# Performance work log

Hardware: AMD Instinct MI355X
Metric: run time of the kernel (lower is better)

## Reference

```python
import jax, jax.numpy as jnp
import numpy as np

BLOCK = 32          # per_1x32 microscaling block size along K
FP4_MAX = 6.0       # largest magnitude representable in e2m1
FP4_EMAX = 2.0      # exponent of largest fp4 binade (4..6)


def _quant_dequant_mxfp4(x):
    """Simulate MXFP4 (e2m1 elements, shared power-of-two E8M0 scale per 1x32
    block along the last dim): quantize then dequantize. x: [..., K], K % 32 == 0."""
    shape = x.shape
    xb = x.reshape(*shape[:-1], shape[-1] // BLOCK, BLOCK)
    amax = jnp.max(jnp.abs(xb), axis=-1, keepdims=True)
    # shared scale: 2^(floor(log2(amax)) - emax) so the block max lands in the top binade
    exp = jnp.floor(jnp.log2(jnp.maximum(amax, jnp.finfo(x.dtype).tiny))) - FP4_EMAX
    scale = jnp.where(amax > 0, jnp.exp2(exp), jnp.ones_like(amax))
    q = jnp.clip(xb / scale, -FP4_MAX, FP4_MAX)
    aq = jnp.abs(q)
    # e2m1 ulp: 0.5 on [0,2), 1 on [2,4), 2 on [4,6]
    lsb = jnp.where(aq < 2.0, 0.5, jnp.where(aq < 4.0, 1.0, 2.0))
    qr = jnp.round(q / lsb) * lsb  # round-to-nearest-even onto the fp4 grid
    return (qr * scale).reshape(shape)


def setup_inputs() -> dict:
    key = jax.random.key(0)
    k1, k2, k3 = jax.random.split(key, 3)
    B, S, K, N = 4, 2048, 2048, 2048
    inp = jax.random.normal(k1, (B, S, K), dtype=jnp.float32)
    weight = jax.random.normal(k2, (N, K), dtype=jnp.float32) * (1.0 / np.sqrt(K))
    bias = jax.random.normal(k3, (N,), dtype=jnp.float32) * 0.02
    return {"input": inp, "weight": weight, "bias": bias}


def reference(input, weight, bias):
    # both activation and weight are fake-quantized to MXFP4 per 1x32 blocks
    # along the contraction (in_features) dim, then a standard GEMM + bias.
    orig_shape = input.shape
    a = _quant_dequant_mxfp4(input.reshape(-1, orig_shape[-1]))  # [M, K]
    w = _quant_dequant_mxfp4(weight)                              # [N, K]
    out = jnp.einsum("mk,nk->mn", a, w) + bias
    return out.reshape(*orig_shape[:-1], weight.shape[0])
```

## Files before the change

### kernel.cpp

```cpp
#include <hip/hip_runtime.h>
#include <hip/hip_bf16.h>
#include <cstdint>


#define BM 128
#define BN 128
#define BKE 256

typedef float floatx4 __attribute__((ext_vector_type(4)));
typedef int intx8 __attribute__((ext_vector_type(8)));

#define GLOBAL_AS __attribute__((address_space(1)))
#define LDS_AS __attribute__((address_space(3)))


__device__ __forceinline__ int enc1(float x, float inv) {
    float q = x * inv;
    q = fminf(fmaxf(q, -6.0f), 6.0f);
    int s = (int)(__float_as_uint(q) >> 31) << 3;
    float aq = fabsf(q);
    float ilsb = aq < 2.0f ? 2.0f : (aq < 4.0f ? 1.0f : 0.5f);
    float lsb  = aq < 2.0f ? 0.5f : (aq < 4.0f ? 1.0f : 2.0f);
    float ar = rintf(aq * ilsb) * lsb;
    int c;
    if (ar < 2.0f)      c = (int)(ar * 2.0f);
    else if (ar < 4.0f) c = 2 + (int)ar;
    else                c = 4 + (int)(ar * 0.5f);
    return c | s;
}

__global__ void quant_mxfp4_v3(const float* __restrict__ A, uint8_t* __restrict__ Aq,
                               uint8_t* __restrict__ Asc,
                               const float* __restrict__ W, uint8_t* __restrict__ Wq,
                               uint8_t* __restrict__ Wsc,
                               long na4, long ntot4) {
    long t = (long)blockIdx.x * 256 + threadIdx.x;
    if (t >= ntot4) return;
    const float* src; uint8_t* dq; uint8_t* ds; long idx;
    if (t < na4) { src = A; dq = Aq; ds = Asc; idx = t; }
    else         { src = W; dq = Wq; ds = Wsc; idx = t - na4; }

    float4 f = ((const float4*)src)[idx];
    float amax = fmaxf(fmaxf(fabsf(f.x), fabsf(f.y)),
                       fmaxf(fabsf(f.z), fabsf(f.w)));
    amax = fmaxf(amax, __shfl_xor(amax, 1));
    amax = fmaxf(amax, __shfl_xor(amax, 2));
    amax = fmaxf(amax, __shfl_xor(amax, 4));

    int ebits = (int)((__float_as_uint(amax) >> 23) & 0xff);
    int sb;
    float inv;
    if (amax > 0.0f) {
        sb = ebits - 2; if (sb < 0) sb = 0;
        inv = __uint_as_float((unsigned)((256 - ebits) & 255) << 23);
    } else {
        sb = 127;
        inv = 0.0f;
    }

    int c0 = enc1(f.x, inv), c1 = enc1(f.y, inv);
    int c2 = enc1(f.z, inv), c3 = enc1(f.w, inv);
    ((unsigned short*)dq)[idx] =
        (unsigned short)(c0 | (c1 << 4) | (c2 << 8) | (c3 << 12));
    if ((idx & 7) == 0) ds[idx >> 3] = (uint8_t)sb;
}


__global__ void gemm_fp4_kernel(const uint8_t* __restrict__ Aq, const uint8_t* __restrict__ Asc,
                                const uint8_t* __restrict__ Wq, const uint8_t* __restrict__ Wsc,
                                const float* __restrict__ bias, float* __restrict__ C,
                                int M, int N, int K) {
    __shared__ __align__(16) uint8_t As4[BM * BKE / 2];
    __shared__ __align__(16) uint8_t Ws4[BN * BKE / 2];
    __shared__ __align__(16) uint8_t SAs[BM * 8];
    __shared__ __align__(16) uint8_t SWs[BN * 8];

    const int tid = threadIdx.x;
    const int lane = tid & 63;
    const int w = tid >> 6;
    const int wr = w >> 1;
    const int wc = w & 1;
    const int row16 = lane & 15;
    const int quad = lane >> 4;
    const int sh = quad * 8;
    const int m0 = blockIdx.y * BM;
    const int n0 = blockIdx.x * BN;
    const int KB2 = K >> 1, KB32 = K >> 5;

    floatx4 acc[4][4];
#pragma unroll
    for (int i = 0; i < 4; i++)
#pragma unroll
        for (int j = 0; j < 4; j++) acc[i][j] = (floatx4){0.f, 0.f, 0.f, 0.f};

    for (int k0 = 0; k0 < K; k0 += BKE) {
#pragma unroll
        for (int it = 0; it < 4; ++it) {
            int q = it * 256 + tid;
            int row = q >> 3, c = q & 7;
            int cg = c ^ (row & 7);
            const uint8_t* ga = Aq + (size_t)(m0 + row) * KB2 + (k0 >> 1) + cg * 16;
            __builtin_amdgcn_global_load_lds(
                (GLOBAL_AS void*)ga, (LDS_AS void*)(As4 + q * 16), 16, 0, 0);
        }
#pragma unroll
        for (int it = 0; it < 4; ++it) {
            int q = it * 256 + tid;
            int row = q >> 3, c = q & 7;
            int cg = c ^ (row & 7);
            const uint8_t* gw = Wq + (size_t)(n0 + row) * KB2 + (k0 >> 1) + cg * 16;
            __builtin_amdgcn_global_load_lds(
                (GLOBAL_AS void*)gw, (LDS_AS void*)(Ws4 + q * 16), 16, 0, 0);
        }
        {
            int row = tid >> 1, half = tid & 1;
            const uint8_t* gsa = Asc + (size_t)(m0 + row) * KB32 + (k0 >> 5) + half * 4;
            __builtin_amdgcn_global_load_lds(
                (GLOBAL_AS void*)gsa, (LDS_AS void*)(SAs + tid * 4), 4, 0, 0);
            const uint8_t* gsw = Wsc + (size_t)(n0 + row) * KB32 + (k0 >> 5) + half * 4;
            __builtin_amdgcn_global_load_lds(
                (GLOBAL_AS void*)gsw, (LDS_AS void*)(SWs + tid * 4), 4, 0, 0);
        }
        __syncthreads();

        uint2 sa2[4], sw2[4];
#pragma unroll
        for (int mi = 0; mi < 4; mi++)
            sa2[mi] = *(const uint2*)(SAs + (wr * 64 + mi * 16 + row16) * 8);
#pragma unroll
        for (int ni = 0; ni < 4; ni++)
            sw2[ni] = *(const uint2*)(SWs + (wc * 64 + ni * 16 + row16) * 8);

#pragma unroll
        for (int ks = 0; ks < 2; ++ks) {
            int4 af[4], wf[4];
#pragma unroll
            for (int mi = 0; mi < 4; mi++) {
                int r = wr * 64 + mi * 16 + row16;
                int c = ((ks * 4 + quad) ^ (r & 7)) * 16;
                af[mi] = *(const int4*)(As4 + r * 128 + c);
            }
#pragma unroll
            for (int ni = 0; ni < 4; ni++) {
                int r = wc * 64 + ni * 16 + row16;
                int c = ((ks * 4 + quad) ^ (r & 7)) * 16;
                wf[ni] = *(const int4*)(Ws4 + r * 128 + c);
            }
            int sas[4], sws[4];
#pragma unroll
            for (int mi = 0; mi < 4; mi++)
                sas[mi] = (int)(((ks ? sa2[mi].y : sa2[mi].x) >> sh) & 0xff);
#pragma unroll
            for (int ni = 0; ni < 4; ni++)
                sws[ni] = (int)(((ks ? sw2[ni].y : sw2[ni].x) >> sh) & 0xff);

#pragma unroll
            for (int mi = 0; mi < 4; mi++) {
                intx8 a8 = {af[mi].x, af[mi].y, af[mi].z, af[mi].w, 0, 0, 0, 0};
#pragma unroll
                for (int ni = 0; ni < 4; ni++) {
                    intx8 b8 = {wf[ni].x, wf[ni].y, wf[ni].z, wf[ni].w, 0, 0, 0, 0};
                    acc[mi][ni] = __builtin_amdgcn_mfma_scale_f32_16x16x128_f8f6f4(
                        a8, b8, acc[mi][ni], 4, 4, 0, sas[mi], 0, sws[ni]);
                }
            }
        }
        __syncthreads();
    }

#pragma unroll
    for (int ni = 0; ni < 4; ni++) {
        int n = n0 + wc * 64 + ni * 16 + row16;
        float bv = bias[n];
#pragma unroll
        for (int mi = 0; mi < 4; mi++) {
            int mbase = m0 + wr * 64 + mi * 16 + quad * 4;
#pragma unroll
            for (int r = 0; r < 4; r++) {
                C[(size_t)(mbase + r) * N + n] = acc[mi][ni][r] + bv;
            }
        }
    }
}


extern "C" void kernel_launch(void* const* d_in, const int* in_sizes, int n_in,
                              void* d_out, int out_size, void* d_ws, size_t ws_size,
                              hipStream_t stream) {
    const float* inp  = (const float*)d_in[0];
    const float* wgt  = (const float*)d_in[1];
    const float* bias = (const float*)d_in[2];
    float* out = (float*)d_out;

    const int N = in_sizes[2];
    const int K = in_sizes[1] / N;
    const long M = (long)in_sizes[0] / K;

    uint8_t* Aq4 = (uint8_t*)d_ws;
    uint8_t* Wq4 = Aq4 + (size_t)M * K / 2;
    uint8_t* Asc = Wq4 + (size_t)N * K / 2;
    uint8_t* Wsc = Asc + (size_t)M * K / 32;

    long na4   = (long)M * K / 4;
    long ntot4 = na4 + (long)N * K / 4;
    quant_mxfp4_v3<<<dim3((ntot4 + 255) / 256), dim3(256), 0, stream>>>(
        inp, Aq4, Asc, wgt, Wq4, Wsc, na4, ntot4);

    dim3 grid(N / BN, M / BM);
    gemm_fp4_kernel<<<grid, dim3(256), 0, stream>>>(
        Aq4, Asc, Wq4, Wsc, bias, out, (int)M, N, K);
}
```

Before: 158.2 us.

## Prepack FP4 operands in MFMA fragment order and load directly without LDS

The quantizer now writes FP4 values and scales in a tiled layout that matches the MFMA 16x16x128 lane order, one 1KB chunk per 16-row by 128-K tile. The GEMM drops shared memory and barriers and has each lane load its fragments and scales straight from global memory with contiguous 16-byte loads. This removes LDS staging and synchronization, but gives up reuse of tiles across waves through LDS. Each wave now reads its A and W tiles from global memory or L2 independently, with no software prefetch or double buffering. The layout math assumes K is a power of two divisible by 512.

```diff
diff --git a/kernel.cpp b/kernel.cpp
--- a/kernel.cpp
+++ b/kernel.cpp
@@ -3,15 +3,8 @@
 #include <cstdint>
 
 
-#define BM 128
-#define BN 128
-#define BKE 256
-
 typedef float floatx4 __attribute__((ext_vector_type(4)));
 typedef int intx8 __attribute__((ext_vector_type(8)));
-
-#define GLOBAL_AS __attribute__((address_space(1)))
-#define LDS_AS __attribute__((address_space(3)))
 
 
 __device__ __forceinline__ int enc1(float x, float inv) {
@@ -29,11 +22,11 @@
     return c | s;
 }
 
-__global__ void quant_mxfp4_v3(const float* __restrict__ A, uint8_t* __restrict__ Aq,
+__global__ void quant_mxfp4_v4(const float* __restrict__ A, uint8_t* __restrict__ Aq,
                                uint8_t* __restrict__ Asc,
                                const float* __restrict__ W, uint8_t* __restrict__ Wq,
                                uint8_t* __restrict__ Wsc,
-                               long na4, long ntot4) {
+                               long na4, long ntot4, int k4shift, int K) {
     long t = (long)blockIdx.x * 256 + threadIdx.x;
     if (t >= ntot4) return;
     const float* src; uint8_t* dq; uint8_t* ds; long idx;
@@ -60,21 +53,31 @@
 
     int c0 = enc1(f.x, inv), c1 = enc1(f.y, inv);
     int c2 = enc1(f.z, inv), c3 = enc1(f.w, inv);
-    ((unsigned short*)dq)[idx] =
+    unsigned short pk =
         (unsigned short)(c0 | (c1 << 4) | (c2 << 8) | (c3 << 12));
-    if ((idx & 7) == 0) ds[idx >> 3] = (uint8_t)sb;
+
+    int m = (int)(idx >> k4shift);
+    int k = (int)(idx & ((1 << k4shift) - 1)) << 2;
+    int KT = K >> 7;
+    int tm = m >> 4, tk = k >> 7;
+    int lane = (((k >> 5) & 3) << 4) | (m & 15);
+    size_t doff = (((size_t)tm * KT + tk) << 10) + (size_t)(lane << 4)
+                + (size_t)(((k & 31) >> 2) << 1);
+    *(unsigned short*)(dq + doff) = pk;
+
+    if ((k & 31) == 0) {
+        int KG = KT >> 2;
+        size_t soff = (((size_t)tm * KG + (tk >> 2)) << 8)
+                    + (size_t)(lane << 2) + (size_t)(tk & 3);
+        ds[soff] = (uint8_t)sb;
+    }
 }
 
 
-__global__ void gemm_fp4_kernel(const uint8_t* __restrict__ Aq, const uint8_t* __restrict__ Asc,
-                                const uint8_t* __restrict__ Wq, const uint8_t* __restrict__ Wsc,
-                                const float* __restrict__ bias, float* __restrict__ C,
-                                int M, int N, int K) {
-    __shared__ __align__(16) uint8_t As4[BM * BKE / 2];
-    __shared__ __align__(16) uint8_t Ws4[BN * BKE / 2];
-    __shared__ __align__(16) uint8_t SAs[BM * 8];
-    __shared__ __align__(16) uint8_t SWs[BN * 8];
-
+__global__ void gemm_fp4_flat(const uint8_t* __restrict__ Aq, const uint8_t* __restrict__ Asc,
+                              const uint8_t* __restrict__ Wq, const uint8_t* __restrict__ Wsc,
+                              const float* __restrict__ bias, float* __restrict__ C,
+                              int M, int N, int K) {
     const int tid = threadIdx.x;
     const int lane = tid & 63;
     const int w = tid >> 6;
@@ -82,10 +85,10 @@
     const int wc = w & 1;
     const int row16 = lane & 15;
     const int quad = lane >> 4;
-    const int sh = quad * 8;
-    const int m0 = blockIdx.y * BM;
-    const int n0 = blockIdx.x * BN;
-    const int KB2 = K >> 1, KB32 = K >> 5;
+    const int m0 = blockIdx.y * 128;
+    const int n0 = blockIdx.x * 128;
+    const int KT = K >> 7;
+    const int KG = KT >> 2;
 
     floatx4 acc[4][4];
 #pragma unroll
@@ -93,79 +96,55 @@
 #pragma unroll
         for (int j = 0; j < 4; j++) acc[i][j] = (floatx4){0.f, 0.f, 0.f, 0.f};
 
-    for (int k0 = 0; k0 < K; k0 += BKE) {
+    const uint8_t* aP[4];
+    const uint8_t* wP[4];
+    const uint8_t* aS[4];
+    const uint8_t* wS[4];
 #pragma unroll
-        for (int it = 0; it < 4; ++it) {
-            int q = it * 256 + tid;
-            int row = q >> 3, c = q & 7;
-            int cg = c ^ (row & 7);
-            const uint8_t* ga = Aq + (size_t)(m0 + row) * KB2 + (k0 >> 1) + cg * 16;
-            __builtin_amdgcn_global_load_lds(
-                (GLOBAL_AS void*)ga, (LDS_AS void*)(As4 + q * 16), 16, 0, 0);
-        }
+    for (int mi = 0; mi < 4; mi++) {
+        int tm = (m0 >> 4) + wr * 4 + mi;
+        aP[mi] = Aq + (((size_t)tm * KT) << 10) + (lane << 4);
+        aS[mi] = Asc + (((size_t)tm * KG) << 8) + (lane << 2);
+    }
 #pragma unroll
-        for (int it = 0; it < 4; ++it) {
-            int q = it * 256 + tid;
-            int row = q >> 3, c = q & 7;
-            int cg = c ^ (row & 7);
-            const uint8_t* gw = Wq + (size_t)(n0 + row) * KB2 + (k0 >> 1) + cg * 16;
-            __builtin_amdgcn_global_load_lds(
-                (GLOBAL_AS void*)gw, (LDS_AS void*)(Ws4 + q * 16), 16, 0, 0);
-        }
-        {
-            int row = tid >> 1, half = tid & 1;
-            const uint8_t* gsa = Asc + (size_t)(m0 + row) * KB32 + (k0 >> 5) + half * 4;
-            __builtin_amdgcn_global_load_lds(
-                (GLOBAL_AS void*)gsa, (LDS_AS void*)(SAs + tid * 4), 4, 0, 0);
-            const uint8_t* gsw = Wsc + (size_t)(n0 + row) * KB32 + (k0 >> 5) + half * 4;
-            __builtin_amdgcn_global_load_lds(
-                (GLOBAL_AS void*)gsw, (LDS_AS void*)(SWs + tid * 4), 4, 0, 0);
-        }
-        __syncthreads();
+    for (int ni = 0; ni < 4; ni++) {
+        int tn = (n0 >> 4) + wc * 4 + ni;
+        wP[ni] = Wq + (((size_t)tn * KT) << 10) + (lane << 4);
+        wS[ni] = Wsc + (((size_t)tn * KG) << 8) + (lane << 2);
+    }
 
-        uint2 sa2[4], sw2[4];
+    for (int g = 0; g < KG; ++g) {
+        unsigned int sa32[4], sw32[4];
 #pragma unroll
         for (int mi = 0; mi < 4; mi++)
-            sa2[mi] = *(const uint2*)(SAs + (wr * 64 + mi * 16 + row16) * 8);
+            sa32[mi] = *(const unsigned int*)(aS[mi] + ((size_t)g << 8));
 #pragma unroll
         for (int ni = 0; ni < 4; ni++)
-            sw2[ni] = *(const uint2*)(SWs + (wc * 64 + ni * 16 + row16) * 8);
+            sw32[ni] = *(const unsigned int*)(wS[ni] + ((size_t)g << 8));
 
 #pragma unroll
-        for (int ks = 0; ks < 2; ++ks) {
+        for (int t = 0; t < 4; ++t) {
             int4 af[4], wf[4];
 #pragma unroll
-            for (int mi = 0; mi < 4; mi++) {
-                int r = wr * 64 + mi * 16 + row16;
-                int c = ((ks * 4 + quad) ^ (r & 7)) * 16;
-                af[mi] = *(const int4*)(As4 + r * 128 + c);
-            }
-#pragma unroll
-            for (int ni = 0; ni < 4; ni++) {
-                int r = wc * 64 + ni * 16 + row16;
-                int c = ((ks * 4 + quad) ^ (r & 7)) * 16;
-                wf[ni] = *(const int4*)(Ws4 + r * 128 + c);
-            }
-            int sas[4], sws[4];
-#pragma unroll
             for (int mi = 0; mi < 4; mi++)
-                sas[mi] = (int)(((ks ? sa2[mi].y : sa2[mi].x) >> sh) & 0xff);
+                af[mi] = *(const int4*)(aP[mi] + ((size_t)(g * 4 + t) << 10));
 #pragma unroll
             for (int ni = 0; ni < 4; ni++)
-                sws[ni] = (int)(((ks ? sw2[ni].y : sw2[ni].x) >> sh) & 0xff);
+                wf[ni] = *(const int4*)(wP[ni] + ((size_t)(g * 4 + t) << 10));
 
 #pragma unroll
             for (int mi = 0; mi < 4; mi++) {
                 intx8 a8 = {af[mi].x, af[mi].y, af[mi].z, af[mi].w, 0, 0, 0, 0};
+                int sa = (int)((sa32[mi] >> (t * 8)) & 0xff);
 #pragma unroll
                 for (int ni = 0; ni < 4; ni++) {
                     intx8 b8 = {wf[ni].x, wf[ni].y, wf[ni].z, wf[ni].w, 0, 0, 0, 0};
+                    int sw = (int)((sw32[ni] >> (t * 8)) & 0xff);
                     acc[mi][ni] = __builtin_amdgcn_mfma_scale_f32_16x16x128_f8f6f4(
-                        a8, b8, acc[mi][ni], 4, 4, 0, sas[mi], 0, sws[ni]);
+                        a8, b8, acc[mi][ni], 4, 4, 0, sa, 0, sw);
                 }
             }
         }
-        __syncthreads();
     }
 
 #pragma unroll
@@ -201,12 +180,15 @@
     uint8_t* Asc = Wq4 + (size_t)N * K / 2;
     uint8_t* Wsc = Asc + (size_t)M * K / 32;
 
+    int k4 = K >> 2;
+    int k4shift = 31 - __builtin_clz((unsigned)k4);
+
     long na4   = (long)M * K / 4;
     long ntot4 = na4 + (long)N * K / 4;
-    quant_mxfp4_v3<<<dim3((ntot4 + 255) / 256), dim3(256), 0, stream>>>(
-        inp, Aq4, Asc, wgt, Wq4, Wsc, na4, ntot4);
+    quant_mxfp4_v4<<<dim3((ntot4 + 255) / 256), dim3(256), 0, stream>>>(
+        inp, Aq4, Asc, wgt, Wq4, Wsc, na4, ntot4, k4shift, K);
 
-    dim3 grid(N / BN, M / BM);
-    gemm_fp4_kernel<<<grid, dim3(256), 0, stream>>>(
+    dim3 grid(N / 128, M / 128);
+    gemm_fp4_flat<<<grid, dim3(256), 0, stream>>>(
         Aq4, Asc, Wq4, Wsc, bias, out, (int)M, N, K);
 }
```

Result: slower. 236.8 us (+49.7%).
